# Performance work log

Hardware: AMD Instinct MI355X
Metric: run time of the kernel (lower is better)

The kernel has to match this reference:

```python
import jax, jax.numpy as jnp
import numpy as np

INPUT_DIM = 512
HIDDEN_DIM = 512


def _linear_params(key, in_dim, out_dim):
    kw, kb = jax.random.split(key)
    bound = 1.0 / np.sqrt(in_dim)
    W = jax.random.uniform(kw, (out_dim, in_dim), minval=-bound, maxval=bound, dtype=jnp.float32)
    b = jax.random.uniform(kb, (out_dim,), minval=-bound, maxval=bound, dtype=jnp.float32)
    return W, b


def setup_inputs() -> dict:
    key = jax.random.key(0)
    keys = jax.random.split(key, 11)
    B = 8192
    inp = {
        "x_t": jax.random.normal(keys[0], (B, INPUT_DIM), dtype=jnp.float32),
        "h_tm1": jax.random.normal(keys[1], (B, HIDDEN_DIM), dtype=jnp.float32),
        "c_tm1": jax.random.normal(keys[2], (B, HIDDEN_DIM), dtype=jnp.float32),
    }
    names = ["f_x", "f_h", "i_x", "i_h", "g_x", "g_h", "o_x", "o_h"]
    for n, k in zip(names, keys[3:]):
        in_dim = INPUT_DIM if n.endswith("_x") else HIDDEN_DIM
        W, b = _linear_params(k, in_dim, HIDDEN_DIM)
        inp[f"W_{n}"] = W
        inp[f"b_{n}"] = b
    return inp


def reference(x_t, h_tm1, c_tm1,
              W_f_x, b_f_x, W_f_h, b_f_h,
              W_i_x, b_i_x, W_i_h, b_i_h,
              W_g_x, b_g_x, W_g_h, b_g_h,
              W_o_x, b_o_x, W_o_h, b_o_h):
    # Stacked weights: [4, H, D] -> einsum over D gives [B, 4, H].
    Wx = jnp.stack([W_f_x, W_g_x, W_i_x, W_o_x])  # [4, H, Din]
    bx = jnp.stack([b_f_x, b_g_x, b_i_x, b_o_x])  # [4, H]
    Wh = jnp.stack([W_f_h, W_g_h, W_i_h, W_o_h])
    bh = jnp.stack([b_f_h, b_g_h, b_i_h, b_o_h])
    pre = (jnp.einsum('bd,ghd->bgh', x_t, Wx) + bx
           + jnp.einsum('bd,ghd->bgh', h_tm1, Wh) + bh)  # [B, 4, H]
    f_t = jax.nn.sigmoid(pre[:, 0])
    g_t = jnp.tanh(pre[:, 1])
    i_t = jax.nn.sigmoid(pre[:, 2])
    o_t = jax.nn.sigmoid(pre[:, 3])
    c_t = f_t * c_tm1 + i_t * g_t
    h_t = o_t * jnp.tanh(c_t)
    return (h_t, c_t)
```

## Files before the change

kernel.cpp:

```cpp
#include <hip/hip_runtime.h>
#include <cstdint>
#include <cstddef>


typedef __attribute__((ext_vector_type(8))) short short8;
typedef __attribute__((ext_vector_type(4))) float floatx4;

#define AS1(p) ((const __attribute__((address_space(1))) void*)(p))
#define AS3(p) ((__attribute__((address_space(3))) void*)(p))

__device__ __forceinline__ unsigned short f2bf(float f) {
  union { float f; unsigned u; } v; v.f = f;
  unsigned u = v.u;
  return (unsigned short)((u + 0x7fffu + ((u >> 16) & 1u)) >> 16);
}

struct PackArgs {
  const float* x; const float* h;
  const float* wx[4]; const float* wh[4];
  const float* bx[4]; const float* bh[4];
  unsigned short* A; unsigned short* B; float* bias;
};

__global__ __launch_bounds__(256) void pack_all_kernel(PackArgs P) {
  const int bid = blockIdx.x;
  if (bid < 8192) {
    int e = (bid * 256 + threadIdx.x) * 4;
    int b = e >> 10, k = e & 1023;
    const float* src = (k < 512) ? (P.x + b * 512 + k)
                                 : (P.h + b * 512 + (k - 512));
    float4 v = *(const float4*)src;
    ushort4 o;
    o.x = f2bf(v.x); o.y = f2bf(v.y); o.z = f2bf(v.z); o.w = f2bf(v.w);
    *(ushort4*)(P.A + e) = o;
  } else {
    int e = ((bid - 8192) * 256 + threadIdx.x) * 4;
    int n = e >> 10, k = e & 1023;
    int g = n >> 9, hh = n & 511;
    const float* src = (k < 512) ? (P.wx[g] + hh * 512 + k)
                                 : (P.wh[g] + hh * 512 + (k - 512));
    float4 v = *(const float4*)src;
    ushort4 o;
    o.x = f2bf(v.x); o.y = f2bf(v.y); o.z = f2bf(v.z); o.w = f2bf(v.w);
    *(ushort4*)(P.B + e) = o;
    if (k == 0) P.bias[n] = P.bx[g][hh] + P.bh[g][hh];
  }
}


#define LDS4(dst, BASEOFF) do {                                   \
    dst[0] = *(const short8*)(smem + (BASEOFF));                  \
    dst[1] = *(const short8*)(smem + (BASEOFF) + 1024);           \
    dst[2] = *(const short8*)(smem + (BASEOFF) + 2048);           \
    dst[3] = *(const short8*)(smem + (BASEOFF) + 3072);           \
  } while (0)

#define MFMA16(MB) do {                                           \
    _Pragma("unroll")                                             \
    for (int i_ = 0; i_ < 4; ++i_)                                \
      _Pragma("unroll")                                           \
      for (int j_ = 0; j_ < 4; ++j_)                              \
        acc[(MB) + i_][j_] = __builtin_amdgcn_mfma_f32_16x16x32_bf16( \
            af[i_], bf[j_], acc[(MB) + i_][j_], 0, 0, 0);         \
  } while (0)

__global__ __launch_bounds__(512, 2)
void lstm_gemm_kernel(const unsigned short* __restrict__ A,
                      const unsigned short* __restrict__ B,
                      const float* __restrict__ bias,
                      const float* __restrict__ c_prev,
                      float* __restrict__ h_out,
                      float* __restrict__ c_out) {
  __shared__ __align__(16) char smem[131072];
  __shared__ float biasS[256];

  const int tid  = threadIdx.x;
  const int lane = tid & 63;
  const int w    = tid >> 6;
  const int quad = lane >> 4;
  const int colA = lane & 15;
  const int m0   = blockIdx.x * 256;
  const int h0   = blockIdx.y * 64;

  if (tid < 256) {
    biasS[tid] = bias[(tid >> 6) * 512 + h0 + (tid & 63)];
  }

  const int wm = (w >> 2) * 128;
  const int wn = (w & 3) * 64;

  const int swzR = (quad ^ ((colA >> 1) & 3)) * 16;
  const int rdA  = (wm + colA) * 64 + swzR;
  const int rdB  = (wn + colA) * 64 + swzR;

  const int lrow   = lane >> 2;
  const int swzS   = ((lane & 3) ^ ((lane >> 3) & 3)) * 16;
  const int sgArow = m0 + w * 32 + lrow;
  const int growB0 = ((2 * w + 0) >> 2) * 512 + h0 + ((w * 32) & 63) + lrow;
  const int growB1 = ((2 * w + 1) >> 2) * 512 + h0 + ((w * 32 + 16) & 63) + lrow;
  const int ldsStage = w * 2048 + lane * 16;

  const char* Ag = (const char*)A;
  const char* Bg = (const char*)B;

  floatx4 acc[8][4];
#pragma unroll
  for (int i = 0; i < 8; ++i)
#pragma unroll
    for (int j = 0; j < 4; ++j) acc[i][j] = (floatx4){0.f, 0.f, 0.f, 0.f};

  auto stageA = [&](int ktt, int kh, int bb) {
    const int kb = (ktt & 15) * 128 + kh * 64;
#pragma unroll
    for (int l = 0; l < 2; ++l)
      __builtin_amdgcn_global_load_lds(
          AS1(Ag + (size_t)(sgArow + l * 16) * 2048 + kb + swzS),
          AS3(smem + bb * 32768 + kh * 16384 + ldsStage + l * 1024), 16, 0, 0);
  };
  auto stageB = [&](int ktt, int kh, int bb) {
    const int kb = (ktt & 15) * 128 + kh * 64;
    __builtin_amdgcn_global_load_lds(
        AS1(Bg + (size_t)growB0 * 2048 + kb + swzS),
        AS3(smem + 65536 + bb * 32768 + kh * 16384 + ldsStage), 16, 0, 0);
    __builtin_amdgcn_global_load_lds(
        AS1(Bg + (size_t)growB1 * 2048 + kb + swzS),
        AS3(smem + 65536 + bb * 32768 + kh * 16384 + ldsStage + 1024), 16, 0, 0);
  };

  stageA(0, 0, 0); stageB(0, 0, 0);
  stageA(0, 1, 0); stageB(0, 1, 0);
  stageA(1, 0, 1); stageB(1, 0, 1);
  asm volatile("s_waitcnt vmcnt(8)" ::: "memory");
  __builtin_amdgcn_s_barrier();
  asm volatile("" ::: "memory");

  short8 af[4], bf[4];

  for (int kt = 0; kt < 16; ++kt) {
    const int buf = kt & 1;
    const int bA  = buf * 32768;
    const int bB  = 65536 + buf * 32768;

    LDS4(af, bA + rdA);
    LDS4(bf, bB + rdB);
    stageA(kt + 1, 1, buf ^ 1);
    __builtin_amdgcn_s_barrier();
    asm volatile("s_waitcnt lgkmcnt(0)" ::: "memory");
    __builtin_amdgcn_s_setprio(1);
    MFMA16(0);
    __builtin_amdgcn_s_setprio(0);
    __builtin_amdgcn_s_barrier();

    LDS4(af, bA + rdA + 4096);
    stageB(kt + 1, 1, buf ^ 1);
    __builtin_amdgcn_s_barrier();
    asm volatile("s_waitcnt lgkmcnt(0)" ::: "memory");
    __builtin_amdgcn_s_setprio(1);
    MFMA16(4);
    __builtin_amdgcn_s_setprio(0);
    asm volatile("s_waitcnt vmcnt(8)" ::: "memory");
    __builtin_amdgcn_s_barrier();
    asm volatile("" ::: "memory");

    LDS4(af, bA + 16384 + rdA);
    LDS4(bf, bB + 16384 + rdB);
    stageA(kt + 2, 0, buf);
    __builtin_amdgcn_s_barrier();
    asm volatile("s_waitcnt lgkmcnt(0)" ::: "memory");
    __builtin_amdgcn_s_setprio(1);
    MFMA16(0);
    __builtin_amdgcn_s_setprio(0);
    __builtin_amdgcn_s_barrier();

    LDS4(af, bA + 16384 + rdA + 4096);
    stageB(kt + 2, 0, buf);
    __builtin_amdgcn_s_barrier();
    asm volatile("s_waitcnt lgkmcnt(0)" ::: "memory");
    __builtin_amdgcn_s_setprio(1);
    MFMA16(4);
    __builtin_amdgcn_s_setprio(0);
    asm volatile("s_waitcnt vmcnt(8)" ::: "memory");
    __builtin_amdgcn_s_barrier();
    asm volatile("" ::: "memory");
  }

  asm volatile("s_waitcnt vmcnt(0)" ::: "memory");
  __syncthreads();

  float* ep = (float*)smem;
  const int gate = w & 3;
#pragma unroll
  for (int rd = 0; rd < 4; ++rd) {
    if ((w >> 2) == (rd >> 1)) {
      const int mib = (rd & 1) * 4;
#pragma unroll
      for (int mi2 = 0; mi2 < 4; ++mi2)
#pragma unroll
        for (int ni = 0; ni < 4; ++ni) {
          int rr0 = mi2 * 16 + quad * 4;
          int cc  = gate * 64 + ni * 16 + colA;
#pragma unroll
          for (int rr = 0; rr < 4; ++rr)
            ep[(rr0 + rr) * 258 + cc] = acc[mib + mi2][ni][rr];
        }
    }
    __syncthreads();
#pragma unroll
    for (int j = 0; j < 8; ++j) {
      int idx  = j * 512 + tid;
      int mloc = idx >> 6;
      int hh   = idx & 63;
      float pf = ep[mloc * 258 +       hh] + biasS[hh];
      float pi = ep[mloc * 258 +  64 + hh] + biasS[64 + hh];
      float pg = ep[mloc * 258 + 128 + hh] + biasS[128 + hh];
      float po = ep[mloc * 258 + 192 + hh] + biasS[192 + hh];
      float fg = 1.f / (1.f + __expf(-pf));
      float ig = 1.f / (1.f + __expf(-pi));
      float gg = 1.f - 2.f / (1.f + __expf(2.f * pg));
      float og = 1.f / (1.f + __expf(-po));
      int m  = m0 + rd * 64 + mloc;
      int hg = h0 + hh;
      float cp = c_prev[m * 512 + hg];
      float cv = fg * cp + ig * gg;
      float th = 1.f - 2.f / (1.f + __expf(2.f * cv));
      h_out[m * 512 + hg] = og * th;
      c_out[m * 512 + hg] = cv;
    }
    __syncthreads();
  }
}

extern "C" void kernel_launch(void* const* d_in, const int* in_sizes, int n_in,
                              void* d_out, int out_size, void* d_ws, size_t ws_size,
                              hipStream_t stream) {
  char* ws = (char*)d_ws;
  unsigned short* Abf = (unsigned short*)ws;
  unsigned short* Bbf = (unsigned short*)(ws + (size_t)16777216);
  float* bias = (float*)(ws + (size_t)16777216 + 4194304);

  float* hout = (float*)d_out;
  float* cout = hout + (size_t)8192 * 512;

  PackArgs P;
  P.x = (const float*)d_in[0];
  P.h = (const float*)d_in[1];
  P.wx[0] = (const float*)d_in[3];  P.bx[0] = (const float*)d_in[4];
  P.wh[0] = (const float*)d_in[5];  P.bh[0] = (const float*)d_in[6];
  P.wx[1] = (const float*)d_in[7];  P.bx[1] = (const float*)d_in[8];
  P.wh[1] = (const float*)d_in[9];  P.bh[1] = (const float*)d_in[10];
  P.wx[2] = (const float*)d_in[11]; P.bx[2] = (const float*)d_in[12];
  P.wh[2] = (const float*)d_in[13]; P.bh[2] = (const float*)d_in[14];
  P.wx[3] = (const float*)d_in[15]; P.bx[3] = (const float*)d_in[16];
  P.wh[3] = (const float*)d_in[17]; P.bh[3] = (const float*)d_in[18];
  P.A = Abf; P.B = Bbf; P.bias = bias;

  pack_all_kernel<<<10240, 256, 0, stream>>>(P);

  const float* c = (const float*)d_in[2];
  dim3 grid(32, 8);
  lstm_gemm_kernel<<<grid, 512, 0, stream>>>(Abf, Bbf, bias, c, hout, cout);
}
```

Before: 178.4 us.

## Restructure LDS tile layout and reorder MFMA quadrants to reuse fragments

The K-tile layout in LDS changes from two 64-wide halves to full 128-byte rows with an 8-way XOR swizzle. Staging is reassigned so each stage call loads half of the M or N rows over the full K tile. The main loop now walks the 8x4 accumulator grid in quadrants in a snake order, so A and B fragments stay in registers across phases. This should cut LDS reads per K-step and spread global loads more evenly across the four phases. The cost is more fragment registers and a different wait/barrier schedule, which could hurt occupancy or correctness if the vmcnt counts are wrong.

```diff
diff --git a/kernel.cpp b/kernel.cpp
--- a/kernel.cpp
+++ b/kernel.cpp
@@ -48,20 +48,17 @@
 }
 
 
-#define LDS4(dst, BASEOFF) do {                                   \
-    dst[0] = *(const short8*)(smem + (BASEOFF));                  \
-    dst[1] = *(const short8*)(smem + (BASEOFF) + 1024);           \
-    dst[2] = *(const short8*)(smem + (BASEOFF) + 2048);           \
-    dst[3] = *(const short8*)(smem + (BASEOFF) + 3072);           \
-  } while (0)
-
-#define MFMA16(MB) do {                                           \
-    _Pragma("unroll")                                             \
-    for (int i_ = 0; i_ < 4; ++i_)                                \
-      _Pragma("unroll")                                           \
-      for (int j_ = 0; j_ < 4; ++j_)                              \
-        acc[(MB) + i_][j_] = __builtin_amdgcn_mfma_f32_16x16x32_bf16( \
-            af[i_], bf[j_], acc[(MB) + i_][j_], 0, 0, 0);         \
+#define MFMA_Q(MB, NB, AF, BF) do {                                    \
+    _Pragma("unroll")                                                  \
+    for (int mi_ = 0; mi_ < 4; ++mi_)                                  \
+      _Pragma("unroll")                                                \
+      for (int ni_ = 0; ni_ < 2; ++ni_)                                \
+        _Pragma("unroll")                                              \
+        for (int kk_ = 0; kk_ < 2; ++kk_)                              \
+          acc[(MB) + mi_][(NB) + ni_] =                                \
+              __builtin_amdgcn_mfma_f32_16x16x32_bf16(                 \
+                  AF[mi_][kk_], BF[ni_][kk_],                          \
+                  acc[(MB) + mi_][(NB) + ni_], 0, 0, 0);               \
   } while (0)
 
 __global__ __launch_bounds__(512, 2)
@@ -89,16 +86,14 @@
   const int wm = (w >> 2) * 128;
   const int wn = (w & 3) * 64;
 
-  const int swzR = (quad ^ ((colA >> 1) & 3)) * 16;
-  const int rdA  = (wm + colA) * 64 + swzR;
-  const int rdB  = (wn + colA) * 64 + swzR;
-
-  const int lrow   = lane >> 2;
-  const int swzS   = ((lane & 3) ^ ((lane >> 3) & 3)) * 16;
-  const int sgArow = m0 + w * 32 + lrow;
-  const int growB0 = ((2 * w + 0) >> 2) * 512 + h0 + ((w * 32) & 63) + lrow;
-  const int growB1 = ((2 * w + 1) >> 2) * 512 + h0 + ((w * 32 + 16) & 63) + lrow;
-  const int ldsStage = w * 2048 + lane * 16;
+  const int swz0 = (quad ^ (colA & 7)) * 16;
+  const int swz1 = swz0 ^ 64;
+  const int aOff = (wm + colA) * 128;
+  const int bOff = (wn + colA) * 128;
+
+  const int sRow   = tid >> 3;
+  const int srcswz = ((tid & 7) ^ ((tid >> 3) & 7)) * 16;
+  const int ldsOff = tid * 16;
 
   const char* Ag = (const char*)A;
   const char* Bg = (const char*)B;
@@ -109,79 +104,88 @@
 #pragma unroll
     for (int j = 0; j < 4; ++j) acc[i][j] = (floatx4){0.f, 0.f, 0.f, 0.f};
 
-  auto stageA = [&](int ktt, int kh, int bb) {
-    const int kb = (ktt & 15) * 128 + kh * 64;
+  auto stageA = [&](int ktt, int hh) {
+    const int kb = (ktt & 15) * 128;
+    const int db = (ktt & 1) * 32768 + hh * 16384 + ldsOff;
 #pragma unroll
     for (int l = 0; l < 2; ++l)
       __builtin_amdgcn_global_load_lds(
-          AS1(Ag + (size_t)(sgArow + l * 16) * 2048 + kb + swzS),
-          AS3(smem + bb * 32768 + kh * 16384 + ldsStage + l * 1024), 16, 0, 0);
+          AS1(Ag + (size_t)(m0 + hh * 128 + l * 64 + sRow) * 2048 + kb + srcswz),
+          AS3(smem + db + l * 8192), 16, 0, 0);
   };
-  auto stageB = [&](int ktt, int kh, int bb) {
-    const int kb = (ktt & 15) * 128 + kh * 64;
-    __builtin_amdgcn_global_load_lds(
-        AS1(Bg + (size_t)growB0 * 2048 + kb + swzS),
-        AS3(smem + 65536 + bb * 32768 + kh * 16384 + ldsStage), 16, 0, 0);
-    __builtin_amdgcn_global_load_lds(
-        AS1(Bg + (size_t)growB1 * 2048 + kb + swzS),
-        AS3(smem + 65536 + bb * 32768 + kh * 16384 + ldsStage + 1024), 16, 0, 0);
+  auto stageB = [&](int ktt, int hh) {
+    const int kb = (ktt & 15) * 128;
+    const int db = 65536 + (ktt & 1) * 32768 + hh * 16384 + ldsOff;
+#pragma unroll
+    for (int l = 0; l < 2; ++l)
+      __builtin_amdgcn_global_load_lds(
+          AS1(Bg + (size_t)((2 * hh + l) * 512 + h0 + sRow) * 2048 + kb + srcswz),
+          AS3(smem + db + l * 8192), 16, 0, 0);
   };
 
-  stageA(0, 0, 0); stageB(0, 0, 0);
-  stageA(0, 1, 0); stageB(0, 1, 0);
-  stageA(1, 0, 1); stageB(1, 0, 1);
-  asm volatile("s_waitcnt vmcnt(8)" ::: "memory");
+  stageB(0, 0); stageA(0, 0); stageB(0, 1); stageA(0, 1);
+  stageB(1, 0); stageA(1, 0);
+  asm volatile("s_waitcnt vmcnt(4)" ::: "memory");
   __builtin_amdgcn_s_barrier();
-  asm volatile("" ::: "memory");
-
-  short8 af[4], bf[4];
+
+  short8 af[4][2], bf[2][2], bf2[2][2];
 
   for (int kt = 0; kt < 16; ++kt) {
-    const int buf = kt & 1;
-    const int bA  = buf * 32768;
-    const int bB  = 65536 + buf * 32768;
-
-    LDS4(af, bA + rdA);
-    LDS4(bf, bB + rdB);
-    stageA(kt + 1, 1, buf ^ 1);
+    const int bA = (kt & 1) * 32768;
+    const int bB = 65536 + (kt & 1) * 32768;
+
+#pragma unroll
+    for (int mi = 0; mi < 4; ++mi) {
+      af[mi][0] = *(const short8*)(smem + bA + aOff + mi * 2048 + swz0);
+      af[mi][1] = *(const short8*)(smem + bA + aOff + mi * 2048 + swz1);
+    }
+#pragma unroll
+    for (int ni = 0; ni < 2; ++ni) {
+      bf[ni][0] = *(const short8*)(smem + bB + bOff + ni * 2048 + swz0);
+      bf[ni][1] = *(const short8*)(smem + bB + bOff + ni * 2048 + swz1);
+    }
+    stageB(kt + 1, 1);
+    asm volatile("s_waitcnt lgkmcnt(8)" ::: "memory");
     __builtin_amdgcn_s_barrier();
     asm volatile("s_waitcnt lgkmcnt(0)" ::: "memory");
     __builtin_amdgcn_s_setprio(1);
-    MFMA16(0);
-    __builtin_amdgcn_s_setprio(0);
-    __builtin_amdgcn_s_barrier();
-
-    LDS4(af, bA + rdA + 4096);
-    stageB(kt + 1, 1, buf ^ 1);
+    MFMA_Q(0, 0, af, bf);
+    __builtin_amdgcn_s_setprio(0);
+    __builtin_amdgcn_s_barrier();
+
+#pragma unroll
+    for (int ni = 0; ni < 2; ++ni) {
+      bf2[ni][0] = *(const short8*)(smem + bB + bOff + (ni + 2) * 2048 + swz0);
+      bf2[ni][1] = *(const short8*)(smem + bB + bOff + (ni + 2) * 2048 + swz1);
+    }
+    stageA(kt + 1, 1);
     __builtin_amdgcn_s_barrier();
     asm volatile("s_waitcnt lgkmcnt(0)" ::: "memory");
     __builtin_amdgcn_s_setprio(1);
-    MFMA16(4);
-    __builtin_amdgcn_s_setprio(0);
-    asm volatile("s_waitcnt vmcnt(8)" ::: "memory");
-    __builtin_amdgcn_s_barrier();
-    asm volatile("" ::: "memory");
-
-    LDS4(af, bA + 16384 + rdA);
-    LDS4(bf, bB + 16384 + rdB);
-    stageA(kt + 2, 0, buf);
+    MFMA_Q(0, 2, af, bf2);
+    __builtin_amdgcn_s_setprio(0);
+    __builtin_amdgcn_s_barrier();
+
+#pragma unroll
+    for (int mi = 0; mi < 4; ++mi) {
+      af[mi][0] = *(const short8*)(smem + bA + aOff + (mi + 4) * 2048 + swz0);
+      af[mi][1] = *(const short8*)(smem + bA + aOff + (mi + 4) * 2048 + swz1);
+    }
+    stageB(kt + 2, 0);
     __builtin_amdgcn_s_barrier();
     asm volatile("s_waitcnt lgkmcnt(0)" ::: "memory");
     __builtin_amdgcn_s_setprio(1);
-    MFMA16(0);
-    __builtin_amdgcn_s_setprio(0);
-    __builtin_amdgcn_s_barrier();
-
-    LDS4(af, bA + 16384 + rdA + 4096);
-    stageB(kt + 2, 0, buf);
-    __builtin_amdgcn_s_barrier();
-    asm volatile("s_waitcnt lgkmcnt(0)" ::: "memory");
-    __builtin_amdgcn_s_setprio(1);
-    MFMA16(4);
-    __builtin_amdgcn_s_setprio(0);
-    asm volatile("s_waitcnt vmcnt(8)" ::: "memory");
-    __builtin_amdgcn_s_barrier();
-    asm volatile("" ::: "memory");
+    MFMA_Q(4, 2, af, bf2);
+    __builtin_amdgcn_s_setprio(0);
+    __builtin_amdgcn_s_barrier();
+
+    stageA(kt + 2, 0);
+    __builtin_amdgcn_s_barrier();
+    __builtin_amdgcn_s_setprio(1);
+    MFMA_Q(4, 0, af, bf);
+    __builtin_amdgcn_s_setprio(0);
+    asm volatile("s_waitcnt vmcnt(4)" ::: "memory");
+    __builtin_amdgcn_s_barrier();
   }
 
   asm volatile("s_waitcnt vmcnt(0)" ::: "memory");
```

Result: faster. 173.9 us (-2.5%).
